# Kernel tuning notes

Measured on AMD Instinct MI355X. Metric: run time of the kernel, lower is better.

Reference implementation:

```python
import jax, jax.numpy as jnp
import numpy as np

N_NODES = 100000
N_EDGES = 1600000
FACTOR = 0.5
REPEAT = 2


def setup_inputs() -> dict:
    key = jax.random.key(0)
    ks = jax.random.split(key, 8)
    x = jax.random.normal(ks[0], (N_NODES, 32), dtype=jnp.float32)
    edge_val = jax.random.uniform(ks[1], (N_EDGES,), dtype=jnp.float32)
    edge_row = jax.random.randint(ks[2], (N_EDGES,), 0, N_NODES)
    edge_col = jax.random.randint(ks[3], (N_EDGES,), 0, N_NODES)
    W1 = jax.random.normal(ks[4], (32, 64), dtype=jnp.float32) * 0.05
    b1 = jnp.zeros((64,), dtype=jnp.float32)
    W2 = jax.random.normal(ks[5], (64, 64), dtype=jnp.float32) * 0.05
    b2 = jnp.zeros((64,), dtype=jnp.float32)
    return {"x": x, "edge_val": edge_val, "edge_row": edge_row,
            "edge_col": edge_col, "W1": W1, "b1": b1, "W2": W2, "b2": b2}


def _spmm(edge_row, edge_col, edge_val, h):
    # out[r] += (factor * val_e) * h[c]  for each edge e=(r,c)
    gathered = (FACTOR * edge_val)[:, None] * h[edge_col]  # [E, D]
    return jax.ops.segment_sum(gathered, edge_row, num_segments=N_NODES)


def _propagate(edge_row, edge_col, edge_val, h):
    # h = (factor*A)^repeat @ h
    for _ in range(REPEAT):
        h = _spmm(edge_row, edge_col, edge_val, h)
    return h


def reference(x, edge_val, edge_row, edge_col, W1, b1, W2, b2):
    # layer 1: propagate -> linear -> relu
    h = _propagate(edge_row, edge_col, edge_val, x)
    h = jax.nn.relu(h @ W1 + b1)
    # layer 2: propagate -> linear -> identity
    h = _propagate(edge_row, edge_col, edge_val, h)
    h = h @ W2 + b2
    return h
```

## Files before the change

### kernel.cpp

```cpp
#include <hip/hip_runtime.h>
#include <hip/hip_bf16.h>


#define REGION_SHIFT 9
#define REGION_SIZE  (1 << REGION_SHIFT)
#define COL_MASK 0x1FFFF
#define GBUILD 256

typedef unsigned short u16;
typedef unsigned int   u32;
typedef __attribute__((ext_vector_type(8))) short bf16x8;
typedef __attribute__((ext_vector_type(4))) float f32x4;

__device__ inline float bflo(u32 w) { return __uint_as_float(w << 16); }
__device__ inline float bfhi(u32 w) { return __uint_as_float(w & 0xffff0000u); }
__device__ inline u32 bfpack(float a, float b) {
    u32 ua = __float_as_uint(a), ub = __float_as_uint(b);
    ua = (ua + 0x7fffu + ((ua >> 16) & 1u)) >> 16;
    ub = (ub + 0x7fffu + ((ub >> 16) & 1u)) & 0xffff0000u;
    return ua | ub;
}
__device__ inline u16 bf1(float f) {
    u32 u = __float_as_uint(f);
    return (u16)((u + 0x7fffu + ((u >> 16) & 1u)) >> 16);
}

__global__ void region_count_kernel(const int* __restrict__ er, int E,
                                    int* __restrict__ partial,
                                    const float* __restrict__ x,
                                    u16* __restrict__ xb, int n4) {
    for (int i = blockIdx.x * 256 + threadIdx.x; i < n4; i += gridDim.x * 256) {
        float4 a = reinterpret_cast<const float4*>(x)[i];
        uint2 o;
        o.x = bfpack(a.x, a.y);
        o.y = bfpack(a.z, a.w);
        reinterpret_cast<uint2*>(xb)[i] = o;
    }
    __shared__ int hist[256];
    int t = threadIdx.x;
    hist[t] = 0;
    __syncthreads();
    int chunk = (E + gridDim.x - 1) / gridDim.x;
    int s = blockIdx.x * chunk;
    int e = min(E, s + chunk);
    for (int i = s + t; i < e; i += 256)
        atomicAdd(&hist[er[i] >> REGION_SHIFT], 1);
    __syncthreads();
    partial[blockIdx.x * 256 + t] = hist[t];
}

__global__ void region_scan_kernel(const int* __restrict__ partial,
                                   int* __restrict__ region_off,
                                   int nreg, int E, int G) {
    __shared__ int s[256];
    int t = threadIdx.x;
    int total = 0;
    if (t < nreg)
        for (int b = 0; b < G; b++) total += partial[b * 256 + t];
    s[t] = (t < nreg) ? total : 0;
    __syncthreads();
    for (int off = 1; off < 256; off <<= 1) {
        int x = (t >= off) ? s[t - off] : 0;
        __syncthreads();
        s[t] += x;
        __syncthreads();
    }
    if (t < nreg) region_off[t] = s[t] - total;
    if (t == 0) region_off[nreg] = E;
}

__global__ void region_base_kernel(int* __restrict__ partial,
                                   const int* __restrict__ region_off, int nreg) {
    __shared__ int s[256];
    int r = blockIdx.x;
    if (r >= nreg) return;
    int t = threadIdx.x;
    int c = partial[t * 256 + r];
    s[t] = c;
    __syncthreads();
    for (int off = 1; off < 256; off <<= 1) {
        int x = (t >= off) ? s[t - off] : 0;
        __syncthreads();
        s[t] += x;
        __syncthreads();
    }
    partial[t * 256 + r] = region_off[r] + s[t] - c;
}

__global__ void coarse_scatter_kernel(const int* __restrict__ er,
                                      const int* __restrict__ ec,
                                      const float* __restrict__ ev, int E,
                                      const int* __restrict__ partial,
                                      int2* __restrict__ stg) {
    __shared__ int cnt2[256], gbase[256];
    int t = threadIdx.x;
    cnt2[t] = 0;
    gbase[t] = partial[blockIdx.x * 256 + t];
    __syncthreads();
    int chunk = (E + gridDim.x - 1) / gridDim.x;
    int s0 = blockIdx.x * chunk;
    int e0 = min(E, s0 + chunk);
    for (int i = s0 + t; i < e0; i += 256) {
        int r = er[i];
        int b = r >> REGION_SHIFT;
        int rank = atomicAdd(&cnt2[b], 1);
        int2 rec;
        rec.x = ec[i] | ((r & (REGION_SIZE - 1)) << 17);
        rec.y = (int)bf1(0.5f * ev[i]);
        stg[gbase[b] + rank] = rec;
    }
}

__global__ void region_sort_kernel(const int2* __restrict__ stg,
                                   const int* __restrict__ region_off,
                                   int* __restrict__ row_ptr,
                                   u32* __restrict__ cv, int N, int E) {
    __shared__ int hist[REGION_SIZE];
    __shared__ int wp_local[REGION_SIZE];
    __shared__ int psum[256];
    int cb = blockIdx.x;
    int lo = cb << REGION_SHIFT;
    if (lo >= N) return;
    int hi = min(lo + REGION_SIZE, N);
    int cnt = hi - lo;
    int t = threadIdx.x;
    for (int r = t; r < cnt; r += 256) hist[r] = 0;
    __syncthreads();
    int start = region_off[cb];
    int end   = region_off[cb + 1];
    for (int q = start + t; q < end; q += 256)
        atomicAdd(&hist[stg[q].x >> 17], 1);
    __syncthreads();
    int a0 = (2 * t     < cnt) ? hist[2 * t]     : 0;
    int a1 = (2 * t + 1 < cnt) ? hist[2 * t + 1] : 0;
    psum[t] = a0 + a1;
    __syncthreads();
    for (int off = 1; off < 256; off <<= 1) {
        int x = (t >= off) ? psum[t - off] : 0;
        __syncthreads();
        psum[t] += x;
        __syncthreads();
    }
    int excl = psum[t] - (a0 + a1);
    if (2 * t < cnt) {
        wp_local[2 * t] = start + excl;
        row_ptr[lo + 2 * t] = start + excl;
    }
    if (2 * t + 1 < cnt) {
        wp_local[2 * t + 1] = start + excl + a0;
        row_ptr[lo + 2 * t + 1] = start + excl + a0;
    }
    if (cb == 0 && t == 0) row_ptr[N] = E;
    __syncthreads();
    for (int q = start + t; q < end; q += 256) {
        int2 e = stg[q];
        int lr = e.x >> 17;
        int p = atomicAdd(&wp_local[lr], 1);
        cv[p] = ((u32)e.y << 17) | ((u32)e.x & COL_MASK);
    }
}

__device__ inline void fma8(float acc[8], float v, uint4 w) {
    acc[0] = fmaf(v, bflo(w.x), acc[0]); acc[1] = fmaf(v, bfhi(w.x), acc[1]);
    acc[2] = fmaf(v, bflo(w.y), acc[2]); acc[3] = fmaf(v, bfhi(w.y), acc[3]);
    acc[4] = fmaf(v, bflo(w.z), acc[4]); acc[5] = fmaf(v, bfhi(w.z), acc[5]);
    acc[6] = fmaf(v, bflo(w.w), acc[6]); acc[7] = fmaf(v, bfhi(w.w), acc[7]);
}
__device__ inline float cvval(u32 q) { return __uint_as_float((q >> 17) << 16); }

template <int D, bool FINAL>
__global__ __launch_bounds__(256) void spmm_bf16_kernel(
        const u16* __restrict__ h,
        const int* __restrict__ row_ptr,
        const u32* __restrict__ cv,
        void* __restrict__ outp,
        const float* __restrict__ bias,
        int N) {
    constexpr int LPR = D / 8;
    int gid = blockIdx.x * 256 + threadIdx.x;
    int row = gid / LPR;
    int sub = gid % LPR;
    if (row >= N) return;
    int start = row_ptr[row];
    int end   = row_ptr[row + 1];
    float acc[8] = {0.f, 0.f, 0.f, 0.f, 0.f, 0.f, 0.f, 0.f};
    int j = start;
    for (; j + 4 <= end; j += 4) {
        u32 q0 = cv[j], q1 = cv[j + 1], q2 = cv[j + 2], q3 = cv[j + 3];
        uint4 w0 = reinterpret_cast<const uint4*>(h + (size_t)(q0 & COL_MASK) * D)[sub];
        uint4 w1 = reinterpret_cast<const uint4*>(h + (size_t)(q1 & COL_MASK) * D)[sub];
        uint4 w2 = reinterpret_cast<const uint4*>(h + (size_t)(q2 & COL_MASK) * D)[sub];
        uint4 w3 = reinterpret_cast<const uint4*>(h + (size_t)(q3 & COL_MASK) * D)[sub];
        fma8(acc, cvval(q0), w0);
        fma8(acc, cvval(q1), w1);
        fma8(acc, cvval(q2), w2);
        fma8(acc, cvval(q3), w3);
    }
    for (; j < end; j++) {
        u32 q = cv[j];
        uint4 w = reinterpret_cast<const uint4*>(h + (size_t)(q & COL_MASK) * D)[sub];
        fma8(acc, cvval(q), w);
    }
    if (FINAL) {
        float* op = (float*)outp + (size_t)row * 64 + sub * 8;
#pragma unroll
        for (int k = 0; k < 8; k++) acc[k] += bias[sub * 8 + k];
        reinterpret_cast<float4*>(op)[0] = make_float4(acc[0], acc[1], acc[2], acc[3]);
        reinterpret_cast<float4*>(op)[1] = make_float4(acc[4], acc[5], acc[6], acc[7]);
    } else {
        u16* ob = (u16*)outp + (size_t)row * D + sub * 8;
        uint4 o;
        o.x = bfpack(acc[0], acc[1]);
        o.y = bfpack(acc[2], acc[3]);
        o.z = bfpack(acc[4], acc[5]);
        o.w = bfpack(acc[6], acc[7]);
        reinterpret_cast<uint4*>(ob)[0] = o;
    }
}

__global__ __launch_bounds__(256) void dense_mfma_kernel(
        const u16* __restrict__ h,
        const float* __restrict__ W1,
        const float* __restrict__ b1,
        const float* __restrict__ W2,
        u16* __restrict__ outb, int N) {
    __shared__ __align__(16) u16 tiles[4][16][80];
    int tid = threadIdx.x;
    int lane = tid & 63;
    int wave = tid >> 6;
    int n16 = lane & 15;
    int quad = lane >> 4;
    u16 (*tile)[80] = tiles[wave];

    int tilebase = (blockIdx.x * 4 + wave) * 16;
    if (tilebase >= N) return;

    bf16x8 w1f[4];
    bf16x8 w2f[4][2];
#pragma unroll
    for (int t = 0; t < 4; t++) {
#pragma unroll
        for (int j = 0; j < 8; j++) {
            int k = quad * 8 + j;
            w1f[t][j] = (short)bf1(W1[k * 64 + t * 16 + n16]);
            w2f[t][0][j] = (short)bf1(W2[k * 64 + t * 16 + n16]);
            w2f[t][1][j] = (short)bf1(W2[(32 + k) * 64 + t * 16 + n16]);
        }
    }
    float b1v[4];
#pragma unroll
    for (int t = 0; t < 4; t++) b1v[t] = b1[t * 16 + n16];

    int arow = min(tilebase + n16, N - 1);
    bf16x8 a1 = *reinterpret_cast<const bf16x8*>(h + (size_t)arow * 32 + quad * 8);
    f32x4 zero = {0.f, 0.f, 0.f, 0.f};
    f32x4 c[4];
#pragma unroll
    for (int t = 0; t < 4; t++)
        c[t] = __builtin_amdgcn_mfma_f32_16x16x32_bf16(a1, w1f[t], zero, 0, 0, 0);

#pragma unroll
    for (int t = 0; t < 4; t++)
#pragma unroll
        for (int i = 0; i < 4; i++)
            tile[quad * 4 + i][t * 16 + n16] = bf1(fmaxf(c[t][i] + b1v[t], 0.f));

    bf16x8 a2_0 = *reinterpret_cast<const bf16x8*>(&tile[n16][quad * 8]);
    bf16x8 a2_1 = *reinterpret_cast<const bf16x8*>(&tile[n16][32 + quad * 8]);
    f32x4 d[4];
#pragma unroll
    for (int t = 0; t < 4; t++) {
        d[t] = __builtin_amdgcn_mfma_f32_16x16x32_bf16(a2_0, w2f[t][0], zero, 0, 0, 0);
        d[t] = __builtin_amdgcn_mfma_f32_16x16x32_bf16(a2_1, w2f[t][1], d[t], 0, 0, 0);
    }

#pragma unroll
    for (int t = 0; t < 4; t++)
#pragma unroll
        for (int i = 0; i < 4; i++)
            tile[quad * 4 + i][t * 16 + n16] = bf1(d[t][i]);

#pragma unroll
    for (int half = 0; half < 2; half++) {
        int g = half * 512 + lane * 8;
        int r = g >> 6, cc = g & 63;
        int grow = tilebase + r;
        if (grow < N)
            *reinterpret_cast<uint4*>(outb + (size_t)grow * 64 + cc) =
                *reinterpret_cast<const uint4*>(&tile[r][cc]);
    }
}

extern "C" void kernel_launch(void* const* d_in, const int* in_sizes, int n_in,
                              void* d_out, int out_size, void* d_ws, size_t ws_size,
                              hipStream_t stream) {
    const float* x        = (const float*)d_in[0];
    const float* edge_val = (const float*)d_in[1];
    const int*   edge_row = (const int*)d_in[2];
    const int*   edge_col = (const int*)d_in[3];
    const float* W1       = (const float*)d_in[4];
    const float* b1       = (const float*)d_in[5];
    const float* W2       = (const float*)d_in[6];
    const float* b2       = (const float*)d_in[7];
    float* out = (float*)d_out;

    const int N = in_sizes[0] / 32;
    const int E = in_sizes[1];
    const int NREG = (N + REGION_SIZE - 1) >> REGION_SHIFT;

    u16* xb  = (u16*)d_out;
    u16* t0b = xb + (size_t)N * 32;
    u16* t2b = (u16*)d_out + (size_t)N * 64;

    u16*  wsb = (u16*)d_ws;
    int2* stg = (int2*)d_ws;
    int*  row_ptr    = (int*)((char*)d_ws + (size_t)N * 64 * 2);
    int*  region_off = row_ptr + (N + 1);
    int*  partial    = region_off + (NREG + 1);
    size_t cvOff = (size_t)((char*)(partial + GBUILD * 256) - (char*)d_ws);
    cvOff = (cvOff + 15) & ~(size_t)15;
    u32* cv = (u32*)((char*)d_ws + cvOff);
    u16* t1b = wsb;
    u16* t3b = wsb;

    int n4 = (N * 32) / 4;

    region_count_kernel<<<GBUILD, 256, 0, stream>>>(edge_row, E, partial, x, xb, n4);
    region_scan_kernel<<<1, 256, 0, stream>>>(partial, region_off, NREG, E, GBUILD);
    region_base_kernel<<<NREG, 256, 0, stream>>>(partial, region_off, NREG);
    coarse_scatter_kernel<<<GBUILD, 256, 0, stream>>>(edge_row, edge_col, edge_val,
                                                      E, partial, stg);
    region_sort_kernel<<<NREG, 256, 0, stream>>>(stg, region_off, row_ptr, cv, N, E);

    int g32 = (N * 4 + 255) / 256;
    int g64 = (N * 8 + 255) / 256;

    spmm_bf16_kernel<32, false><<<g32, 256, 0, stream>>>(xb, row_ptr, cv, t0b, nullptr, N);
    spmm_bf16_kernel<32, false><<<g32, 256, 0, stream>>>(t0b, row_ptr, cv, t1b, nullptr, N);
    dense_mfma_kernel<<<(N + 63) / 64, 256, 0, stream>>>(t1b, W1, b1, W2, t2b, N);
    spmm_bf16_kernel<64, false><<<g64, 256, 0, stream>>>(t2b, row_ptr, cv, t3b, nullptr, N);
    spmm_bf16_kernel<64, true><<<g64, 256, 0, stream>>>(t3b, row_ptr, cv, out, b2, N);
}
```

Baseline: 302.5 us.

## Replace region-sort CSR build with global atomic count/scan/scatter and fuse spmm into dense

```diff
diff --git a/kernel.cpp b/kernel.cpp
--- a/kernel.cpp
+++ b/kernel.cpp
@@ -5,7 +5,6 @@
 #define REGION_SHIFT 9
 #define REGION_SIZE  (1 << REGION_SHIFT)
 #define COL_MASK 0x1FFFF
-#define GBUILD 256
 
 typedef unsigned short u16;
 typedef unsigned int   u32;
@@ -25,114 +24,63 @@
     return (u16)((u + 0x7fffu + ((u >> 16) & 1u)) >> 16);
 }
 
-__global__ void region_count_kernel(const int* __restrict__ er, int E,
-                                    int* __restrict__ partial,
-                                    const float* __restrict__ x,
-                                    u16* __restrict__ xb, int n4) {
-    for (int i = blockIdx.x * 256 + threadIdx.x; i < n4; i += gridDim.x * 256) {
+__global__ void convert_kernel(const float* __restrict__ x,
+                               u16* __restrict__ xb, int n4,
+                               int* __restrict__ rcnt, int N,
+                               const float* __restrict__ W1,
+                               const float* __restrict__ W2,
+                               u16* __restrict__ W1f, u16* __restrict__ W2f) {
+    int tid0 = blockIdx.x * 256 + threadIdx.x;
+    int stride = gridDim.x * 256;
+    for (int i = tid0; i < n4; i += stride) {
         float4 a = reinterpret_cast<const float4*>(x)[i];
         uint2 o;
         o.x = bfpack(a.x, a.y);
         o.y = bfpack(a.z, a.w);
         reinterpret_cast<uint2*>(xb)[i] = o;
     }
-    __shared__ int hist[256];
+    for (int i = tid0; i < N; i += stride) rcnt[i] = 0;
+    if (blockIdx.x == 0) {
+        for (int idx = threadIdx.x; idx < 2048; idx += 256) {
+            int j = idx & 7, n16 = (idx >> 3) & 15;
+            int quad = (idx >> 7) & 3, t = (idx >> 9) & 3;
+            W1f[idx] = bf1(W1[(quad * 8 + j) * 64 + t * 16 + n16]);
+        }
+        for (int idx = threadIdx.x; idx < 4096; idx += 256) {
+            int j = idx & 7, n16 = (idx >> 3) & 15;
+            int quad = (idx >> 7) & 3, half = (idx >> 9) & 1, t = (idx >> 10) & 3;
+            W2f[idx] = bf1(W2[(half * 32 + quad * 8 + j) * 64 + t * 16 + n16]);
+        }
+    }
+}
+
+__global__ void count_kernel(const int* __restrict__ er, int E,
+                             int* __restrict__ rcnt) {
+    for (int i = blockIdx.x * 256 + threadIdx.x; i < E; i += gridDim.x * 256)
+        atomicAdd(&rcnt[er[i]], 1);
+}
+
+__global__ void row_scan_kernel(const int* __restrict__ rcnt,
+                                int* __restrict__ row_ptr,
+                                int* __restrict__ wp, int N, int E) {
+    __shared__ int psum[256];
+    int r = blockIdx.x;
+    int lo = r << REGION_SHIFT;
+    if (lo >= N) return;
+    int cnt = min(N - lo, REGION_SIZE);
     int t = threadIdx.x;
-    hist[t] = 0;
+    int acc = 0;
+    for (int i = t; i < lo; i += 256) acc += rcnt[i];
+    psum[t] = acc;
     __syncthreads();
-    int chunk = (E + gridDim.x - 1) / gridDim.x;
-    int s = blockIdx.x * chunk;
-    int e = min(E, s + chunk);
-    for (int i = s + t; i < e; i += 256)
-        atomicAdd(&hist[er[i] >> REGION_SHIFT], 1);
+    for (int off = 128; off > 0; off >>= 1) {
+        if (t < off) psum[t] += psum[t + off];
+        __syncthreads();
+    }
+    int base = psum[0];
     __syncthreads();
-    partial[blockIdx.x * 256 + t] = hist[t];
-}
-
-__global__ void region_scan_kernel(const int* __restrict__ partial,
-                                   int* __restrict__ region_off,
-                                   int nreg, int E, int G) {
-    __shared__ int s[256];
-    int t = threadIdx.x;
-    int total = 0;
-    if (t < nreg)
-        for (int b = 0; b < G; b++) total += partial[b * 256 + t];
-    s[t] = (t < nreg) ? total : 0;
-    __syncthreads();
-    for (int off = 1; off < 256; off <<= 1) {
-        int x = (t >= off) ? s[t - off] : 0;
-        __syncthreads();
-        s[t] += x;
-        __syncthreads();
-    }
-    if (t < nreg) region_off[t] = s[t] - total;
-    if (t == 0) region_off[nreg] = E;
-}
-
-__global__ void region_base_kernel(int* __restrict__ partial,
-                                   const int* __restrict__ region_off, int nreg) {
-    __shared__ int s[256];
-    int r = blockIdx.x;
-    if (r >= nreg) return;
-    int t = threadIdx.x;
-    int c = partial[t * 256 + r];
-    s[t] = c;
-    __syncthreads();
-    for (int off = 1; off < 256; off <<= 1) {
-        int x = (t >= off) ? s[t - off] : 0;
-        __syncthreads();
-        s[t] += x;
-        __syncthreads();
-    }
-    partial[t * 256 + r] = region_off[r] + s[t] - c;
-}
-
-__global__ void coarse_scatter_kernel(const int* __restrict__ er,
-                                      const int* __restrict__ ec,
-                                      const float* __restrict__ ev, int E,
-                                      const int* __restrict__ partial,
-                                      int2* __restrict__ stg) {
-    __shared__ int cnt2[256], gbase[256];
-    int t = threadIdx.x;
-    cnt2[t] = 0;
-    gbase[t] = partial[blockIdx.x * 256 + t];
-    __syncthreads();
-    int chunk = (E + gridDim.x - 1) / gridDim.x;
-    int s0 = blockIdx.x * chunk;
-    int e0 = min(E, s0 + chunk);
-    for (int i = s0 + t; i < e0; i += 256) {
-        int r = er[i];
-        int b = r >> REGION_SHIFT;
-        int rank = atomicAdd(&cnt2[b], 1);
-        int2 rec;
-        rec.x = ec[i] | ((r & (REGION_SIZE - 1)) << 17);
-        rec.y = (int)bf1(0.5f * ev[i]);
-        stg[gbase[b] + rank] = rec;
-    }
-}
-
-__global__ void region_sort_kernel(const int2* __restrict__ stg,
-                                   const int* __restrict__ region_off,
-                                   int* __restrict__ row_ptr,
-                                   u32* __restrict__ cv, int N, int E) {
-    __shared__ int hist[REGION_SIZE];
-    __shared__ int wp_local[REGION_SIZE];
-    __shared__ int psum[256];
-    int cb = blockIdx.x;
-    int lo = cb << REGION_SHIFT;
-    if (lo >= N) return;
-    int hi = min(lo + REGION_SIZE, N);
-    int cnt = hi - lo;
-    int t = threadIdx.x;
-    for (int r = t; r < cnt; r += 256) hist[r] = 0;
-    __syncthreads();
-    int start = region_off[cb];
-    int end   = region_off[cb + 1];
-    for (int q = start + t; q < end; q += 256)
-        atomicAdd(&hist[stg[q].x >> 17], 1);
-    __syncthreads();
-    int a0 = (2 * t     < cnt) ? hist[2 * t]     : 0;
-    int a1 = (2 * t + 1 < cnt) ? hist[2 * t + 1] : 0;
+    int a0 = (2 * t     < cnt) ? rcnt[lo + 2 * t]     : 0;
+    int a1 = (2 * t + 1 < cnt) ? rcnt[lo + 2 * t + 1] : 0;
     psum[t] = a0 + a1;
     __syncthreads();
     for (int off = 1; off < 256; off <<= 1) {
@@ -141,22 +89,20 @@
         psum[t] += x;
         __syncthreads();
     }
-    int excl = psum[t] - (a0 + a1);
-    if (2 * t < cnt) {
-        wp_local[2 * t] = start + excl;
-        row_ptr[lo + 2 * t] = start + excl;
-    }
-    if (2 * t + 1 < cnt) {
-        wp_local[2 * t + 1] = start + excl + a0;
-        row_ptr[lo + 2 * t + 1] = start + excl + a0;
-    }
-    if (cb == 0 && t == 0) row_ptr[N] = E;
-    __syncthreads();
-    for (int q = start + t; q < end; q += 256) {
-        int2 e = stg[q];
-        int lr = e.x >> 17;
-        int p = atomicAdd(&wp_local[lr], 1);
-        cv[p] = ((u32)e.y << 17) | ((u32)e.x & COL_MASK);
+    int excl = base + psum[t] - (a0 + a1);
+    if (2 * t < cnt)     { row_ptr[lo + 2 * t]     = excl;      wp[lo + 2 * t]     = excl; }
+    if (2 * t + 1 < cnt) { row_ptr[lo + 2 * t + 1] = excl + a0; wp[lo + 2 * t + 1] = excl + a0; }
+    if (r == 0 && t == 0) row_ptr[N] = E;
+}
+
+__global__ void scatter_kernel(const int* __restrict__ er,
+                               const int* __restrict__ ec,
+                               const float* __restrict__ ev, int E,
+                               int* __restrict__ wp, u32* __restrict__ cv) {
+    for (int i = blockIdx.x * 256 + threadIdx.x; i < E; i += gridDim.x * 256) {
+        int r = er[i];
+        int p = atomicAdd(&wp[r], 1);
+        cv[p] = ((u32)bf1(0.5f * ev[i]) << 17) | ((u32)ec[i] & COL_MASK);
     }
 }
 
@@ -218,41 +164,72 @@
     }
 }
 
-__global__ __launch_bounds__(256) void dense_mfma_kernel(
+__global__ __launch_bounds__(256) void spmm_dense_kernel(
         const u16* __restrict__ h,
-        const float* __restrict__ W1,
+        const int* __restrict__ row_ptr,
+        const u32* __restrict__ cv,
+        const u16* __restrict__ W1f,
         const float* __restrict__ b1,
-        const float* __restrict__ W2,
-        u16* __restrict__ outb, int N) {
+        const u16* __restrict__ W2f,
+        u16* __restrict__ outb,
+        int N) {
     __shared__ __align__(16) u16 tiles[4][16][80];
     int tid = threadIdx.x;
     int lane = tid & 63;
     int wave = tid >> 6;
+    int tilebase = blockIdx.x * 64 + wave * 16;
+    if (tilebase >= N) return;
+    int gid = blockIdx.x * 256 + tid;
+    int row = gid >> 2;
+    int sub = gid & 3;
+
+    bool vr = row < N;
+    int start = vr ? row_ptr[row] : 0;
+    int end   = vr ? row_ptr[row + 1] : 0;
+    float acc[8] = {0.f, 0.f, 0.f, 0.f, 0.f, 0.f, 0.f, 0.f};
+    int j = start;
+    for (; j + 4 <= end; j += 4) {
+        u32 q0 = cv[j], q1 = cv[j + 1], q2 = cv[j + 2], q3 = cv[j + 3];
+        uint4 w0 = reinterpret_cast<const uint4*>(h + (size_t)(q0 & COL_MASK) * 32)[sub];
+        uint4 w1 = reinterpret_cast<const uint4*>(h + (size_t)(q1 & COL_MASK) * 32)[sub];
+        uint4 w2 = reinterpret_cast<const uint4*>(h + (size_t)(q2 & COL_MASK) * 32)[sub];
+        uint4 w3 = reinterpret_cast<const uint4*>(h + (size_t)(q3 & COL_MASK) * 32)[sub];
+        fma8(acc, cvval(q0), w0);
+        fma8(acc, cvval(q1), w1);
+        fma8(acc, cvval(q2), w2);
+        fma8(acc, cvval(q3), w3);
+    }
+    for (; j < end; j++) {
+        u32 q = cv[j];
+        uint4 w = reinterpret_cast<const uint4*>(h + (size_t)(q & COL_MASK) * 32)[sub];
+        fma8(acc, cvval(q), w);
+    }
+
+    u16 (*tile)[80] = tiles[wave];
+    {
+        uint4 o;
+        o.x = bfpack(acc[0], acc[1]);
+        o.y = bfpack(acc[2], acc[3]);
+        o.z = bfpack(acc[4], acc[5]);
+        o.w = bfpack(acc[6], acc[7]);
+        *reinterpret_cast<uint4*>(&tile[lane >> 2][sub * 8]) = o;
+    }
+
     int n16 = lane & 15;
     int quad = lane >> 4;
-    u16 (*tile)[80] = tiles[wave];
-
-    int tilebase = (blockIdx.x * 4 + wave) * 16;
-    if (tilebase >= N) return;
-
     bf16x8 w1f[4];
     bf16x8 w2f[4][2];
 #pragma unroll
     for (int t = 0; t < 4; t++) {
-#pragma unroll
-        for (int j = 0; j < 8; j++) {
-            int k = quad * 8 + j;
-            w1f[t][j] = (short)bf1(W1[k * 64 + t * 16 + n16]);
-            w2f[t][0][j] = (short)bf1(W2[k * 64 + t * 16 + n16]);
-            w2f[t][1][j] = (short)bf1(W2[(32 + k) * 64 + t * 16 + n16]);
-        }
+        w1f[t] = *reinterpret_cast<const bf16x8*>(&W1f[((t * 4 + quad) * 16 + n16) * 8]);
+        w2f[t][0] = *reinterpret_cast<const bf16x8*>(&W2f[(((t * 2 + 0) * 4 + quad) * 16 + n16) * 8]);
+        w2f[t][1] = *reinterpret_cast<const bf16x8*>(&W2f[(((t * 2 + 1) * 4 + quad) * 16 + n16) * 8]);
     }
     float b1v[4];
 #pragma unroll
     for (int t = 0; t < 4; t++) b1v[t] = b1[t * 16 + n16];
 
-    int arow = min(tilebase + n16, N - 1);
-    bf16x8 a1 = *reinterpret_cast<const bf16x8*>(h + (size_t)arow * 32 + quad * 8);
+    bf16x8 a1 = *reinterpret_cast<const bf16x8*>(&tile[n16][quad * 8]);
     f32x4 zero = {0.f, 0.f, 0.f, 0.f};
     f32x4 c[4];
 #pragma unroll
@@ -312,32 +289,28 @@
     u16* t0b = xb + (size_t)N * 32;
     u16* t2b = (u16*)d_out + (size_t)N * 64;
 
-    u16*  wsb = (u16*)d_ws;
-    int2* stg = (int2*)d_ws;
-    int*  row_ptr    = (int*)((char*)d_ws + (size_t)N * 64 * 2);
-    int*  region_off = row_ptr + (N + 1);
-    int*  partial    = region_off + (NREG + 1);
-    size_t cvOff = (size_t)((char*)(partial + GBUILD * 256) - (char*)d_ws);
-    cvOff = (cvOff + 15) & ~(size_t)15;
+    u16* t3b = (u16*)d_ws;
+    int* row_ptr = (int*)((char*)d_ws + (size_t)N * 64 * 2);
+    int* wp      = row_ptr + (N + 1);
+    int* rcnt    = wp + N;
+    size_t wOff = (((size_t)((char*)(rcnt + N) - (char*)d_ws)) + 15) & ~(size_t)15;
+    u16* W1f = (u16*)((char*)d_ws + wOff);
+    u16* W2f = W1f + 2048;
+    size_t cvOff = (((size_t)((char*)(W2f + 4096) - (char*)d_ws)) + 15) & ~(size_t)15;
     u32* cv = (u32*)((char*)d_ws + cvOff);
-    u16* t1b = wsb;
-    u16* t3b = wsb;
 
     int n4 = (N * 32) / 4;
 
-    region_count_kernel<<<GBUILD, 256, 0, stream>>>(edge_row, E, partial, x, xb, n4);
-    region_scan_kernel<<<1, 256, 0, stream>>>(partial, region_off, NREG, E, GBUILD);
-    region_base_kernel<<<NREG, 256, 0, stream>>>(partial, region_off, NREG);
-    coarse_scatter_kernel<<<GBUILD, 256, 0, stream>>>(edge_row, edge_col, edge_val,
-                                                      E, partial, stg);
-    region_sort_kernel<<<NREG, 256, 0, stream>>>(stg, region_off, row_ptr, cv, N, E);
+    convert_kernel<<<1024, 256, 0, stream>>>(x, xb, n4, rcnt, N, W1, W2, W1f, W2f);
+    count_kernel<<<2048, 256, 0, stream>>>(edge_row, E, rcnt);
+    row_scan_kernel<<<NREG, 256, 0, stream>>>(rcnt, row_ptr, wp, N, E);
+    scatter_kernel<<<2048, 256, 0, stream>>>(edge_row, edge_col, edge_val, E, wp, cv);
 
     int g32 = (N * 4 + 255) / 256;
     int g64 = (N * 8 + 255) / 256;
 
     spmm_bf16_kernel<32, false><<<g32, 256, 0, stream>>>(xb, row_ptr, cv, t0b, nullptr, N);
-    spmm_bf16_kernel<32, false><<<g32, 256, 0, stream>>>(t0b, row_ptr, cv, t1b, nullptr, N);
-    dense_mfma_kernel<<<(N + 63) / 64, 256, 0, stream>>>(t1b, W1, b1, W2, t2b, N);
+    spmm_dense_kernel<<<g32, 256, 0, stream>>>(t0b, row_ptr, cv, W1f, b1, W2f, t2b, N);
     spmm_bf16_kernel<64, false><<<g64, 256, 0, stream>>>(t2b, row_ptr, cv, t3b, nullptr, N);
     spmm_bf16_kernel<64, true><<<g64, 256, 0, stream>>>(t3b, row_ptr, cv, out, b2, N);
 }
```

Result: slower. 430.8 us (+42.4%).

## Fuse second layer-1 SpMM into dense MFMA kernel and prepack weight fragments

Applied to the files above, without the earlier changes.

```diff
diff --git a/kernel.cpp b/kernel.cpp
--- a/kernel.cpp
+++ b/kernel.cpp
@@ -28,13 +28,29 @@
 __global__ void region_count_kernel(const int* __restrict__ er, int E,
                                     int* __restrict__ partial,
                                     const float* __restrict__ x,
-                                    u16* __restrict__ xb, int n4) {
+                                    u16* __restrict__ xb, int n4,
+                                    const float* __restrict__ W1,
+                                    const float* __restrict__ W2,
+                                    u16* __restrict__ W1f,
+                                    u16* __restrict__ W2f) {
     for (int i = blockIdx.x * 256 + threadIdx.x; i < n4; i += gridDim.x * 256) {
         float4 a = reinterpret_cast<const float4*>(x)[i];
         uint2 o;
         o.x = bfpack(a.x, a.y);
         o.y = bfpack(a.z, a.w);
         reinterpret_cast<uint2*>(xb)[i] = o;
+    }
+    if (blockIdx.x == 0) {
+        for (int idx = threadIdx.x; idx < 2048; idx += 256) {
+            int j = idx & 7, n16 = (idx >> 3) & 15;
+            int quad = (idx >> 7) & 3, t = (idx >> 9) & 3;
+            W1f[idx] = bf1(W1[(quad * 8 + j) * 64 + t * 16 + n16]);
+        }
+        for (int idx = threadIdx.x; idx < 4096; idx += 256) {
+            int j = idx & 7, n16 = (idx >> 3) & 15;
+            int quad = (idx >> 7) & 3, half = (idx >> 9) & 1, t = (idx >> 10) & 3;
+            W2f[idx] = bf1(W2[(half * 32 + quad * 8 + j) * 64 + t * 16 + n16]);
+        }
     }
     __shared__ int hist[256];
     int t = threadIdx.x;
@@ -218,41 +234,72 @@
     }
 }
 
-__global__ __launch_bounds__(256) void dense_mfma_kernel(
+__global__ __launch_bounds__(256) void spmm_dense_kernel(
         const u16* __restrict__ h,
-        const float* __restrict__ W1,
+        const int* __restrict__ row_ptr,
+        const u32* __restrict__ cv,
+        const u16* __restrict__ W1f,
         const float* __restrict__ b1,
-        const float* __restrict__ W2,
-        u16* __restrict__ outb, int N) {
+        const u16* __restrict__ W2f,
+        u16* __restrict__ outb,
+        int N) {
     __shared__ __align__(16) u16 tiles[4][16][80];
     int tid = threadIdx.x;
     int lane = tid & 63;
     int wave = tid >> 6;
+    int tilebase = blockIdx.x * 64 + wave * 16;
+    if (tilebase >= N) return;
+    int gid = blockIdx.x * 256 + tid;
+    int row = gid >> 2;
+    int sub = gid & 3;
+
+    bool vr = row < N;
+    int start = vr ? row_ptr[row] : 0;
+    int end   = vr ? row_ptr[row + 1] : 0;
+    float acc[8] = {0.f, 0.f, 0.f, 0.f, 0.f, 0.f, 0.f, 0.f};
+    int j = start;
+    for (; j + 4 <= end; j += 4) {
+        u32 q0 = cv[j], q1 = cv[j + 1], q2 = cv[j + 2], q3 = cv[j + 3];
+        uint4 w0 = reinterpret_cast<const uint4*>(h + (size_t)(q0 & COL_MASK) * 32)[sub];
+        uint4 w1 = reinterpret_cast<const uint4*>(h + (size_t)(q1 & COL_MASK) * 32)[sub];
+        uint4 w2 = reinterpret_cast<const uint4*>(h + (size_t)(q2 & COL_MASK) * 32)[sub];
+        uint4 w3 = reinterpret_cast<const uint4*>(h + (size_t)(q3 & COL_MASK) * 32)[sub];
+        fma8(acc, cvval(q0), w0);
+        fma8(acc, cvval(q1), w1);
+        fma8(acc, cvval(q2), w2);
+        fma8(acc, cvval(q3), w3);
+    }
+    for (; j < end; j++) {
+        u32 q = cv[j];
+        uint4 w = reinterpret_cast<const uint4*>(h + (size_t)(q & COL_MASK) * 32)[sub];
+        fma8(acc, cvval(q), w);
+    }
+
+    u16 (*tile)[80] = tiles[wave];
+    {
+        uint4 o;
+        o.x = bfpack(acc[0], acc[1]);
+        o.y = bfpack(acc[2], acc[3]);
+        o.z = bfpack(acc[4], acc[5]);
+        o.w = bfpack(acc[6], acc[7]);
+        *reinterpret_cast<uint4*>(&tile[lane >> 2][sub * 8]) = o;
+    }
+
     int n16 = lane & 15;
     int quad = lane >> 4;
-    u16 (*tile)[80] = tiles[wave];
-
-    int tilebase = (blockIdx.x * 4 + wave) * 16;
-    if (tilebase >= N) return;
-
     bf16x8 w1f[4];
     bf16x8 w2f[4][2];
 #pragma unroll
     for (int t = 0; t < 4; t++) {
-#pragma unroll
-        for (int j = 0; j < 8; j++) {
-            int k = quad * 8 + j;
-            w1f[t][j] = (short)bf1(W1[k * 64 + t * 16 + n16]);
-            w2f[t][0][j] = (short)bf1(W2[k * 64 + t * 16 + n16]);
-            w2f[t][1][j] = (short)bf1(W2[(32 + k) * 64 + t * 16 + n16]);
-        }
+        w1f[t] = *reinterpret_cast<const bf16x8*>(&W1f[((t * 4 + quad) * 16 + n16) * 8]);
+        w2f[t][0] = *reinterpret_cast<const bf16x8*>(&W2f[(((t * 2 + 0) * 4 + quad) * 16 + n16) * 8]);
+        w2f[t][1] = *reinterpret_cast<const bf16x8*>(&W2f[(((t * 2 + 1) * 4 + quad) * 16 + n16) * 8]);
     }
     float b1v[4];
 #pragma unroll
     for (int t = 0; t < 4; t++) b1v[t] = b1[t * 16 + n16];
 
-    int arow = min(tilebase + n16, N - 1);
-    bf16x8 a1 = *reinterpret_cast<const bf16x8*>(h + (size_t)arow * 32 + quad * 8);
+    bf16x8 a1 = *reinterpret_cast<const bf16x8*>(&tile[n16][quad * 8]);
     f32x4 zero = {0.f, 0.f, 0.f, 0.f};
     f32x4 c[4];
 #pragma unroll
@@ -312,20 +359,21 @@
     u16* t0b = xb + (size_t)N * 32;
     u16* t2b = (u16*)d_out + (size_t)N * 64;
 
-    u16*  wsb = (u16*)d_ws;
+    u16*  t3b = (u16*)d_ws;
     int2* stg = (int2*)d_ws;
     int*  row_ptr    = (int*)((char*)d_ws + (size_t)N * 64 * 2);
     int*  region_off = row_ptr + (N + 1);
     int*  partial    = region_off + (NREG + 1);
-    size_t cvOff = (size_t)((char*)(partial + GBUILD * 256) - (char*)d_ws);
-    cvOff = (cvOff + 15) & ~(size_t)15;
+    size_t wOff = (((size_t)((char*)(partial + GBUILD * 256) - (char*)d_ws)) + 15) & ~(size_t)15;
+    u16* W1f = (u16*)((char*)d_ws + wOff);
+    u16* W2f = W1f + 2048;
+    size_t cvOff = (((size_t)((char*)(W2f + 4096) - (char*)d_ws)) + 15) & ~(size_t)15;
     u32* cv = (u32*)((char*)d_ws + cvOff);
-    u16* t1b = wsb;
-    u16* t3b = wsb;
 
     int n4 = (N * 32) / 4;
 
-    region_count_kernel<<<GBUILD, 256, 0, stream>>>(edge_row, E, partial, x, xb, n4);
+    region_count_kernel<<<GBUILD, 256, 0, stream>>>(edge_row, E, partial, x, xb, n4,
+                                                    W1, W2, W1f, W2f);
     region_scan_kernel<<<1, 256, 0, stream>>>(partial, region_off, NREG, E, GBUILD);
     region_base_kernel<<<NREG, 256, 0, stream>>>(partial, region_off, NREG);
     coarse_scatter_kernel<<<GBUILD, 256, 0, stream>>>(edge_row, edge_col, edge_val,
@@ -336,8 +384,7 @@
     int g64 = (N * 8 + 255) / 256;
 
     spmm_bf16_kernel<32, false><<<g32, 256, 0, stream>>>(xb, row_ptr, cv, t0b, nullptr, N);
-    spmm_bf16_kernel<32, false><<<g32, 256, 0, stream>>>(t0b, row_ptr, cv, t1b, nullptr, N);
-    dense_mfma_kernel<<<(N + 63) / 64, 256, 0, stream>>>(t1b, W1, b1, W2, t2b, N);
+    spmm_dense_kernel<<<g32, 256, 0, stream>>>(t0b, row_ptr, cv, W1f, b1, W2f, t2b, N);
     spmm_bf16_kernel<64, false><<<g64, 256, 0, stream>>>(t2b, row_ptr, cv, t3b, nullptr, N);
     spmm_bf16_kernel<64, true><<<g64, 256, 0, stream>>>(t3b, row_ptr, cv, out, b2, N);
 }
```

Result: no change. 298.2 us (-1.4%).
